# Kernel tuning notes

Hardware: AMD Instinct MI355X
Metric: run time of the kernel (lower is better)

## Reference

```python
import jax, jax.numpy as jnp
import numpy as np


def setup_inputs() -> dict:
    key = jax.random.key(0)
    x = jax.random.normal(key, (4, 4096, 64), dtype=jnp.float32)
    return {"x": x}


def reference(x) -> jnp.ndarray:
    # self-attention with q = k = v = x, shape [B, S, D]
    d = x.shape[-1]
    scale = 1.0 / jnp.sqrt(jnp.asarray(d, dtype=x.dtype))
    logits = jnp.einsum('bqd,bkd->bqk', x, x) * scale  # [B, S, S]
    attn = jax.nn.softmax(logits, axis=-1)
    return jnp.einsum('bqk,bkd->bqd', attn, x)
```

## Files before the change

kernel.cpp:

```cpp
#include <hip/hip_runtime.h>
#include <cstdint>


#define SB 4096
#define DDIM 64

typedef __attribute__((ext_vector_type(16))) float f32x16;
typedef __attribute__((ext_vector_type(8)))  float f32x8;
typedef __attribute__((ext_vector_type(4)))  float f32x4;
typedef __attribute__((ext_vector_type(8)))  short bf16x8;

static __device__ __forceinline__ unsigned short bf16_rne(float f) {
  union { float f; uint32_t u; } v; v.f = f;
  uint32_t u = v.u + 0x7FFFu + ((v.u >> 16) & 1u);
  return (unsigned short)(u >> 16);
}
static __device__ __forceinline__ float bf16_tof(unsigned short h) {
  union { uint32_t u; float f; } v; v.u = ((uint32_t)h) << 16;
  return v.f;
}
static __device__ __forceinline__ f32x16 MFMA(bf16x8 a, bf16x8 b, f32x16 c) {
  return __builtin_amdgcn_mfma_f32_32x32x16_bf16(a, b, c, 0, 0, 0);
}

#define KF_BYTES  (4u << 20)
#define VT_BYTES  (2u << 20)
#define WS_NEEDED (8u << 20)

__device__ __constant__ int g_koff[16] = {0,1,2,3, 8,9,10,11, 4,5,6,7, 12,13,14,15};

__global__ __launch_bounds__(256)
void precompute_kernel(const float* __restrict__ x, char* __restrict__ ws) {
  const int bid = blockIdx.x;
  const int tid = threadIdx.x;
  char* __restrict__ kfmt = ws;
  char* __restrict__ vthi = ws + KF_BYTES;
  char* __restrict__ vtlo = ws + KF_BYTES + VT_BYTES;
  if (bid < 512) {
    const int t   = bid * 256 + tid;
    const int row = t >> 3;
    const int seg = t & 7;
    f32x8 v = *(const f32x8*)(x + (size_t)row * 64 + seg * 8);
    bf16x8 h, l;
#pragma unroll
    for (int j = 0; j < 8; ++j) {
      unsigned short hi = bf16_rne(v[j]);
      h[j] = (short)hi;
      l[j] = (short)bf16_rne(v[j] - bf16_tof(hi));
    }
    char* dst = kfmt + (size_t)row * 256 + seg * 16;
    *(bf16x8*)dst         = h;
    *(bf16x8*)(dst + 128) = l;
  } else {
    const int w = (bid - 512) * 4 + (tid >> 6);
    const int b = w >> 8;
    const int c = w & 255;
    const int d = tid & 63;
    unsigned short hs[16], ls[16];
#pragma unroll
    for (int s = 0; s < 16; ++s) {
      const int k = c * 16 + g_koff[s];
      float v = x[((size_t)(b * SB + k)) * 64 + d];
      hs[s] = bf16_rne(v);
      ls[s] = bf16_rne(v - bf16_tof(hs[s]));
    }
    bf16x8 h0, h1, l0, l1;
#pragma unroll
    for (int j = 0; j < 8; ++j) {
      h0[j] = (short)hs[j];     h1[j] = (short)hs[j + 8];
      l0[j] = (short)ls[j];     l1[j] = (short)ls[j + 8];
    }
    char* dh = vthi + (size_t)(b * 64 + d) * 8192 + c * 32;
    char* dl = vtlo + (size_t)(b * 64 + d) * 8192 + c * 32;
    *(bf16x8*)dh = h0; *(bf16x8*)(dh + 16) = h1;
    *(bf16x8*)dl = l0; *(bf16x8*)(dl + 16) = l1;
  }
}

__global__ __launch_bounds__(512, 2)
void sdpa_main(const float* __restrict__ x, const char* __restrict__ ws,
               float* __restrict__ out) {
  __shared__ __align__(16) char smem[121856];
  const int tid  = threadIdx.x;
  const int wv   = tid >> 6;
  const int lane = tid & 63;
  const int l31  = lane & 31;
  const int h5   = lane >> 5;

  const int p    = blockIdx.x;
  const int xcd  = p & 7;
  const int slot = p >> 3;
  const int b    = xcd >> 1;
  const int q0   = ((xcd & 1) * 32 + slot) * 64;

  const float* __restrict__ xb = x + (size_t)b * (SB * DDIM);
  const char* __restrict__ kfmt = ws;
  const char* __restrict__ vthi = ws + KF_BYTES;
  const char* __restrict__ vtlo = ws + KF_BYTES + VT_BYTES;

  const float NEG = -3.0e38f;

  bf16x8 qh[2][4], ql[2][4];
#pragma unroll
  for (int qf = 0; qf < 2; ++qf) {
#pragma unroll
    for (int dc = 0; dc < 4; ++dc) {
      const float* ptr = xb + (size_t)(q0 + qf * 32 + l31) * DDIM + dc * 16 + h5 * 8;
      f32x4 a = *(const f32x4*)ptr;
      f32x4 c = *(const f32x4*)(ptr + 4);
      float v[8] = {a[0], a[1], a[2], a[3], c[0], c[1], c[2], c[3]};
#pragma unroll
      for (int j = 0; j < 8; ++j) {
        float sv = v[j] * 0.125f;
        unsigned short hi = bf16_rne(sv);
        qh[qf][dc][j] = (short)hi;
        ql[qf][dc][j] = (short)bf16_rne(sv - bf16_tof(hi));
      }
    }
  }

  f32x16 ot[2][2] = {};
  float mrun[2] = {NEG, NEG};
  float lrun[2] = {0.f, 0.f};

  const int kv0 = wv * (SB / 8);

  const char* kbase = kfmt + (size_t)(b * SB + kv0 + l31) * 256 + h5 * 16;
  const char* vbh   = vthi + (size_t)(b * 64 + l31) * 8192 + (size_t)kv0 * 2 + h5 * 16;
  const char* vbl   = vtlo + (size_t)(b * 64 + l31) * 8192 + (size_t)kv0 * 2 + h5 * 16;

#pragma unroll 1
  for (int st = 0; st < 16; ++st) {
    bf16x8 kh[4], kl[4];
#pragma unroll
    for (int dc = 0; dc < 4; ++dc) {
      kh[dc] = *(const bf16x8*)(kbase + dc * 32);
      kl[dc] = *(const bf16x8*)(kbase + 128 + dc * 32);
    }

    f32x16 s0 = {}, s1 = {};
#pragma unroll
    for (int dc = 0; dc < 4; ++dc) {
      s0 = MFMA(kh[dc], qh[0][dc], s0);
      s1 = MFMA(kh[dc], qh[1][dc], s1);
      s0 = MFMA(kh[dc], ql[0][dc], s0);
      s1 = MFMA(kh[dc], ql[1][dc], s1);
      s0 = MFMA(kl[dc], qh[0][dc], s0);
      s1 = MFMA(kl[dc], qh[1][dc], s1);
    }

    bf16x8 vh[2][2], vl[2][2];
#pragma unroll
    for (int df = 0; df < 2; ++df)
#pragma unroll
      for (int c = 0; c < 2; ++c) {
        vh[df][c] = *(const bf16x8*)(vbh + (size_t)df * (32 * 8192) + c * 32);
        vl[df][c] = *(const bf16x8*)(vbl + (size_t)df * (32 * 8192) + c * 32);
      }

    bf16x8 ph[2][2], pl[2][2];
#pragma unroll
    for (int qf = 0; qf < 2; ++qf) {
      f32x16 sv = qf ? s1 : s0;
      float pm = sv[0];
#pragma unroll
      for (int r = 1; r < 16; ++r) pm = fmaxf(pm, sv[r]);
      pm = fmaxf(pm, __shfl_xor(pm, 32));
      const float mnew = fmaxf(mrun[qf], pm);
      const float corr = __expf(mrun[qf] - mnew);
      mrun[qf] = mnew;
      lrun[qf] *= corr;
#pragma unroll
      for (int df = 0; df < 2; ++df)
#pragma unroll
        for (int r = 0; r < 16; ++r) ot[qf][df][r] *= corr;
      float pv[16]; float ps = 0.f;
#pragma unroll
      for (int r = 0; r < 16; ++r) { pv[r] = __expf(sv[r] - mnew); ps += pv[r]; }
      lrun[qf] += ps;
#pragma unroll
      for (int c = 0; c < 2; ++c)
#pragma unroll
        for (int j = 0; j < 8; ++j) {
          float pvv = pv[c * 8 + j];
          unsigned short hi = bf16_rne(pvv);
          ph[qf][c][j] = (short)hi;
          pl[qf][c][j] = (short)bf16_rne(pvv - bf16_tof(hi));
        }
    }

#pragma unroll
    for (int df = 0; df < 2; ++df)
#pragma unroll
      for (int qf = 0; qf < 2; ++qf)
#pragma unroll
        for (int c = 0; c < 2; ++c) {
          ot[qf][df] = MFMA(vh[df][c], ph[qf][c], ot[qf][df]);
          ot[qf][df] = MFMA(vh[df][c], pl[qf][c], ot[qf][df]);
          ot[qf][df] = MFMA(vl[df][c], ph[qf][c], ot[qf][df]);
        }

    kbase += 32 * 256;
    vbh   += 64;
    vbl   += 64;
  }

#pragma unroll
  for (int qf = 0; qf < 2; ++qf) lrun[qf] += __shfl_xor(lrun[qf], 32);

  __syncthreads();
  if (wv > 0) {
    char* rbase = smem + (size_t)(wv - 1) * 17408 + (size_t)lane * 272;
#pragma unroll
    for (int qf = 0; qf < 2; ++qf)
#pragma unroll
      for (int df = 0; df < 2; ++df)
#pragma unroll
        for (int t = 0; t < 4; ++t) {
          f32x4 o = { ot[qf][df][t*4+0], ot[qf][df][t*4+1],
                      ot[qf][df][t*4+2], ot[qf][df][t*4+3] };
          *(f32x4*)(rbase + (qf * 128 + df * 64 + t * 16)) = o;
        }
    f32x4 stv = { mrun[0], lrun[0], mrun[1], lrun[1] };
    *(f32x4*)(rbase + 256) = stv;
  }
  __syncthreads();
  if (wv == 0) {
#pragma unroll 1
    for (int w = 1; w < 8; ++w) {
      char* rbase = smem + (size_t)(w - 1) * 17408 + (size_t)lane * 272;
      f32x4 stv = *(f32x4*)(rbase + 256);
#pragma unroll
      for (int qf = 0; qf < 2; ++qf) {
        const float mw = stv[qf * 2 + 0];
        const float lw = stv[qf * 2 + 1];
        const float mn = fmaxf(mrun[qf], mw);
        const float f0 = __expf(mrun[qf] - mn);
        const float f1 = __expf(mw - mn);
        mrun[qf] = mn;
        lrun[qf] = lrun[qf] * f0 + lw * f1;
#pragma unroll
        for (int df = 0; df < 2; ++df)
#pragma unroll
          for (int t = 0; t < 4; ++t) {
            f32x4 o = *(f32x4*)(rbase + (qf * 128 + df * 64 + t * 16));
#pragma unroll
            for (int e = 0; e < 4; ++e)
              ot[qf][df][t*4+e] = ot[qf][df][t*4+e] * f0 + o[e] * f1;
          }
      }
    }
#pragma unroll
    for (int qf = 0; qf < 2; ++qf) {
      const float inv = 1.0f / lrun[qf];
      const size_t rowoff = ((size_t)b * SB + q0 + qf * 32 + l31) * DDIM;
#pragma unroll
      for (int df = 0; df < 2; ++df)
#pragma unroll
        for (int t = 0; t < 4; ++t) {
          const int dbase = df * 32 + t * 8 + h5 * 4;
          f32x4 o = { ot[qf][df][t*4+0] * inv, ot[qf][df][t*4+1] * inv,
                      ot[qf][df][t*4+2] * inv, ot[qf][df][t*4+3] * inv };
          *(f32x4*)(out + rowoff + dbase) = o;
        }
    }
  }
}

#define KSTRIDE 272
#define VSTRIDE 144
#define VOFF    8704
#define WREG    17920

__global__ __launch_bounds__(512, 1)
void sdpa_fb(const float* __restrict__ x, float* __restrict__ out) {
  __shared__ __align__(16) char smem[143360];
  const int tid  = threadIdx.x;
  const int wv   = tid >> 6;
  const int lane = tid & 63;
  const int l31  = lane & 31;
  const int h5   = lane >> 5;
  const int bid  = blockIdx.x;
  const int b    = bid >> 6;
  const int q0   = (bid & 63) << 6;
  const float* __restrict__ xb = x + (size_t)b * (SB * DDIM);
  char* __restrict__ wl = smem + (size_t)wv * WREG;
  const float NEG = -3.0e38f;

  bf16x8 qh[2][4], ql[2][4];
#pragma unroll
  for (int qf = 0; qf < 2; ++qf)
#pragma unroll
    for (int dc = 0; dc < 4; ++dc) {
      const float* ptr = xb + (size_t)(q0 + qf * 32 + l31) * DDIM + dc * 16 + h5 * 8;
      f32x4 a = *(const f32x4*)ptr;
      f32x4 c = *(const f32x4*)(ptr + 4);
      float v[8] = {a[0], a[1], a[2], a[3], c[0], c[1], c[2], c[3]};
#pragma unroll
      for (int j = 0; j < 8; ++j) {
        float sv = v[j] * 0.125f;
        unsigned short hi = bf16_rne(sv);
        qh[qf][dc][j] = (short)hi;
        ql[qf][dc][j] = (short)bf16_rne(sv - bf16_tof(hi));
      }
    }

  f32x16 ot[2][2] = {};
  float mrun[2] = {NEG, NEG};
  float lrun[2] = {0.f, 0.f};
  const int kv0 = wv * (SB / 8);
  const int r0  = (lane >> 3) * 4;
  const int d0g = (lane & 7) * 8;
  const int vc  = r0 >> 4;
  const int vko = r0 & 15;
  const int vsA = ((vko >> 2) & 1) * 8 + ((vko >> 3) & 1) * 4;
  const uint32_t vcolb = (uint32_t)(vc * 16 + vsA) * 2;

#pragma unroll 1
  for (int st = 0; st < 16; ++st) {
    const int krow0 = kv0 + st * 32;
    bf16x8 hv[4], lv[4];
#pragma unroll
    for (int i = 0; i < 4; ++i) {
      f32x8 t = *(const f32x8*)(xb + (size_t)(krow0 + r0 + i) * DDIM + d0g);
#pragma unroll
      for (int j = 0; j < 8; ++j) {
        unsigned short hi = bf16_rne(t[j]);
        hv[i][j] = (short)hi;
        lv[i][j] = (short)bf16_rne(t[j] - bf16_tof(hi));
      }
      const int row = r0 + i;
      *(bf16x8*)(wl + row * KSTRIDE + d0g * 2)       = hv[i];
      *(bf16x8*)(wl + row * KSTRIDE + 128 + d0g * 2) = lv[i];
    }
#pragma unroll
    for (int dd = 0; dd < 8; ++dd) {
      const int d = d0g + dd;
      const uint32_t sw = ((uint32_t)((d >> 3) & 7)) << 4;
      char* rb = wl + VOFF + (uint32_t)d * VSTRIDE;
      short4 pa = make_short4(hv[0][dd], hv[1][dd], hv[2][dd], hv[3][dd]);
      short4 pb = make_short4(lv[0][dd], lv[1][dd], lv[2][dd], lv[3][dd]);
      *(short4*)(rb + (vcolb ^ sw))        = pa;
      *(short4*)(rb + ((64 + vcolb) ^ sw)) = pb;
    }

    bf16x8 kh[4], kl[4];
    {
      char* krow = wl + l31 * KSTRIDE;
#pragma unroll
      for (int dc = 0; dc < 4; ++dc) {
        const uint32_t off = (uint32_t)(dc * 32 + h5 * 16);
        kh[dc] = *(bf16x8*)(krow + off);
        kl[dc] = *(bf16x8*)(krow + 128 + off);
      }
    }
    f32x16 s0 = {}, s1 = {};
#pragma unroll
    for (int dc = 0; dc < 4; ++dc) {
      s0 = MFMA(kh[dc], qh[0][dc], s0);
      s1 = MFMA(kh[dc], qh[1][dc], s1);
      s0 = MFMA(kh[dc], ql[0][dc], s0);
      s1 = MFMA(kh[dc], ql[1][dc], s1);
      s0 = MFMA(kl[dc], qh[0][dc], s0);
      s1 = MFMA(kl[dc], qh[1][dc], s1);
    }

    bf16x8 ph[2][2], pl[2][2];
#pragma unroll
    for (int qf = 0; qf < 2; ++qf) {
      f32x16 sv = qf ? s1 : s0;
      float pm = sv[0];
#pragma unroll
      for (int r = 1; r < 16; ++r) pm = fmaxf(pm, sv[r]);
      pm = fmaxf(pm, __shfl_xor(pm, 32));
      const float mnew = fmaxf(mrun[qf], pm);
      const float corr = __expf(mrun[qf] - mnew);
      mrun[qf] = mnew;
      lrun[qf] *= corr;
#pragma unroll
      for (int df = 0; df < 2; ++df)
#pragma unroll
        for (int r = 0; r < 16; ++r) ot[qf][df][r] *= corr;
      float pv[16]; float ps = 0.f;
#pragma unroll
      for (int r = 0; r < 16; ++r) { pv[r] = __expf(sv[r] - mnew); ps += pv[r]; }
      lrun[qf] += ps;
#pragma unroll
      for (int c = 0; c < 2; ++c)
#pragma unroll
        for (int j = 0; j < 8; ++j) {
          float pvv = pv[c * 8 + j];
          unsigned short hi = bf16_rne(pvv);
          ph[qf][c][j] = (short)hi;
          pl[qf][c][j] = (short)bf16_rne(pvv - bf16_tof(hi));
        }
    }

#pragma unroll
    for (int df = 0; df < 2; ++df) {
      const int d = df * 32 + l31;
      char* rb = wl + VOFF + (uint32_t)d * VSTRIDE;
      const uint32_t sw = ((uint32_t)((d >> 3) & 7)) << 4;
      bf16x8 vh[2], vl2[2];
#pragma unroll
      for (int c = 0; c < 2; ++c) {
        const uint32_t off = (uint32_t)(c * 32 + h5 * 16);
        vh[c]  = *(bf16x8*)(rb + (off ^ sw));
        vl2[c] = *(bf16x8*)(rb + ((64 + off) ^ sw));
      }
#pragma unroll
      for (int qf = 0; qf < 2; ++qf)
#pragma unroll
        for (int c = 0; c < 2; ++c) {
          ot[qf][df] = MFMA(vh[c],  ph[qf][c], ot[qf][df]);
          ot[qf][df] = MFMA(vh[c],  pl[qf][c], ot[qf][df]);
          ot[qf][df] = MFMA(vl2[c], ph[qf][c], ot[qf][df]);
        }
    }
  }

#pragma unroll
  for (int qf = 0; qf < 2; ++qf) lrun[qf] += __shfl_xor(lrun[qf], 32);

  __syncthreads();
  if (wv > 0) {
    char* rbase = smem + (size_t)(wv - 1) * 17408 + (size_t)lane * 272;
#pragma unroll
    for (int qf = 0; qf < 2; ++qf)
#pragma unroll
      for (int df = 0; df < 2; ++df)
#pragma unroll
        for (int t = 0; t < 4; ++t) {
          f32x4 o = { ot[qf][df][t*4+0], ot[qf][df][t*4+1],
                      ot[qf][df][t*4+2], ot[qf][df][t*4+3] };
          *(f32x4*)(rbase + (qf * 128 + df * 64 + t * 16)) = o;
        }
    f32x4 stv = { mrun[0], lrun[0], mrun[1], lrun[1] };
    *(f32x4*)(rbase + 256) = stv;
  }
  __syncthreads();
  if (wv == 0) {
#pragma unroll 1
    for (int w = 1; w < 8; ++w) {
      char* rbase = smem + (size_t)(w - 1) * 17408 + (size_t)lane * 272;
      f32x4 stv = *(f32x4*)(rbase + 256);
#pragma unroll
      for (int qf = 0; qf < 2; ++qf) {
        const float mw = stv[qf * 2 + 0];
        const float lw = stv[qf * 2 + 1];
        const float mn = fmaxf(mrun[qf], mw);
        const float f0 = __expf(mrun[qf] - mn);
        const float f1 = __expf(mw - mn);
        mrun[qf] = mn;
        lrun[qf] = lrun[qf] * f0 + lw * f1;
#pragma unroll
        for (int df = 0; df < 2; ++df)
#pragma unroll
          for (int t = 0; t < 4; ++t) {
            f32x4 o = *(f32x4*)(rbase + (qf * 128 + df * 64 + t * 16));
#pragma unroll
            for (int e = 0; e < 4; ++e)
              ot[qf][df][t*4+e] = ot[qf][df][t*4+e] * f0 + o[e] * f1;
          }
      }
    }
#pragma unroll
    for (int qf = 0; qf < 2; ++qf) {
      const float inv = 1.0f / lrun[qf];
      const size_t rowoff = ((size_t)b * SB + q0 + qf * 32 + l31) * DDIM;
#pragma unroll
      for (int df = 0; df < 2; ++df)
#pragma unroll
        for (int t = 0; t < 4; ++t) {
          const int dbase = df * 32 + t * 8 + h5 * 4;
          f32x4 o = { ot[qf][df][t*4+0] * inv, ot[qf][df][t*4+1] * inv,
                      ot[qf][df][t*4+2] * inv, ot[qf][df][t*4+3] * inv };
          *(f32x4*)(out + rowoff + dbase) = o;
        }
    }
  }
}

extern "C" void kernel_launch(void* const* d_in, const int* in_sizes, int n_in,
                              void* d_out, int out_size, void* d_ws, size_t ws_size,
                              hipStream_t stream) {
  (void)in_sizes; (void)n_in; (void)out_size;
  const float* x = (const float*)d_in[0];
  float* o = (float*)d_out;
  if (ws_size >= (size_t)WS_NEEDED) {
    precompute_kernel<<<dim3(768), dim3(256), 0, stream>>>(x, (char*)d_ws);
    sdpa_main<<<dim3(256), dim3(512), 0, stream>>>(x, (const char*)d_ws, o);
  } else {
    sdpa_fb<<<dim3(256), dim3(512), 0, stream>>>(x, o);
  }
}
```

Baseline: 129.1 us.

## Halve per-block query tile, double grid, prefetch K and tree-reduce partials

Each block now handles 32 queries instead of 64, so the grid doubles to 512 blocks, with a smaller LDS footprint and launch bounds allowing 4 blocks per CU. This is meant to raise occupancy and let more waves hide memory latency. The main loop now prefetches the next K-hi tile, splits the score MFMAs across two accumulators, and skips the rescale when no row max changes. The cross-wave merge becomes a tree reduction in shared memory. In exchange, K/V data is reread by twice as many blocks, and the block-to-XCD mapping changes.

```diff
diff --git a/kernel.cpp b/kernel.cpp
--- a/kernel.cpp
+++ b/kernel.cpp
@@ -77,21 +77,20 @@
   }
 }
 
-__global__ __launch_bounds__(512, 2)
+__global__ __launch_bounds__(512, 4)
 void sdpa_main(const float* __restrict__ x, const char* __restrict__ ws,
                float* __restrict__ out) {
-  __shared__ __align__(16) char smem[121856];
+  __shared__ __align__(16) char smem[40960];
   const int tid  = threadIdx.x;
   const int wv   = tid >> 6;
   const int lane = tid & 63;
   const int l31  = lane & 31;
   const int h5   = lane >> 5;
 
-  const int p    = blockIdx.x;
-  const int xcd  = p & 7;
-  const int slot = p >> 3;
-  const int b    = xcd >> 1;
-  const int q0   = ((xcd & 1) * 32 + slot) * 64;
+  const int p  = blockIdx.x;
+  const int b  = (p >> 1) & 3;
+  const int qt = ((p & 1) << 6) | (p >> 3);
+  const int q0 = qt * 32;
 
   const float* __restrict__ xb = x + (size_t)b * (SB * DDIM);
   const char* __restrict__ kfmt = ws;
@@ -100,169 +99,201 @@
 
   const float NEG = -3.0e38f;
 
-  bf16x8 qh[2][4], ql[2][4];
-#pragma unroll
-  for (int qf = 0; qf < 2; ++qf) {
-#pragma unroll
-    for (int dc = 0; dc < 4; ++dc) {
-      const float* ptr = xb + (size_t)(q0 + qf * 32 + l31) * DDIM + dc * 16 + h5 * 8;
-      f32x4 a = *(const f32x4*)ptr;
-      f32x4 c = *(const f32x4*)(ptr + 4);
-      float v[8] = {a[0], a[1], a[2], a[3], c[0], c[1], c[2], c[3]};
-#pragma unroll
-      for (int j = 0; j < 8; ++j) {
-        float sv = v[j] * 0.125f;
-        unsigned short hi = bf16_rne(sv);
-        qh[qf][dc][j] = (short)hi;
-        ql[qf][dc][j] = (short)bf16_rne(sv - bf16_tof(hi));
-      }
-    }
-  }
-
-  f32x16 ot[2][2] = {};
-  float mrun[2] = {NEG, NEG};
-  float lrun[2] = {0.f, 0.f};
-
-  const int kv0 = wv * (SB / 8);
-
-  const char* kbase = kfmt + (size_t)(b * SB + kv0 + l31) * 256 + h5 * 16;
-  const char* vbh   = vthi + (size_t)(b * 64 + l31) * 8192 + (size_t)kv0 * 2 + h5 * 16;
-  const char* vbl   = vtlo + (size_t)(b * 64 + l31) * 8192 + (size_t)kv0 * 2 + h5 * 16;
+  bf16x8 qh[4], ql[4];
+#pragma unroll
+  for (int dc = 0; dc < 4; ++dc) {
+    const float* ptr = xb + (size_t)(q0 + l31) * DDIM + dc * 16 + h5 * 8;
+    f32x4 a = *(const f32x4*)ptr;
+    f32x4 c = *(const f32x4*)(ptr + 4);
+    float v[8] = {a[0], a[1], a[2], a[3], c[0], c[1], c[2], c[3]};
+#pragma unroll
+    for (int j = 0; j < 8; ++j) {
+      float sv = v[j] * 0.125f;
+      unsigned short hi = bf16_rne(sv);
+      qh[dc][j] = (short)hi;
+      ql[dc][j] = (short)bf16_rne(sv - bf16_tof(hi));
+    }
+  }
+
+  f32x16 ot0 = {}, ot1 = {};
+  float mrun = NEG, lrun = 0.f;
+
+  const int kv0 = wv * 512;
+  const int koffl = l31 * 256 + h5 * 16;
+  const int voffl = l31 * 8192 + h5 * 16;
+  const char* kstep = kfmt + (size_t)(b * SB + kv0) * 256;
+  const char* vhs   = vthi + (size_t)(b * 64) * 8192 + kv0 * 2;
+  const char* vls   = vtlo + (size_t)(b * 64) * 8192 + kv0 * 2;
+
+  bf16x8 kh[4], kl[4];
+#pragma unroll
+  for (int dc = 0; dc < 4; ++dc)
+    kh[dc] = *(const bf16x8*)(kstep + koffl + dc * 32);
 
 #pragma unroll 1
   for (int st = 0; st < 16; ++st) {
-    bf16x8 kh[4], kl[4];
+#pragma unroll
+    for (int dc = 0; dc < 4; ++dc)
+      kl[dc] = *(const bf16x8*)(kstep + koffl + 128 + dc * 32);
+
+    f32x16 sa = {}, sb = {};
 #pragma unroll
     for (int dc = 0; dc < 4; ++dc) {
-      kh[dc] = *(const bf16x8*)(kbase + dc * 32);
-      kl[dc] = *(const bf16x8*)(kbase + 128 + dc * 32);
-    }
-
-    f32x16 s0 = {}, s1 = {};
-#pragma unroll
-    for (int dc = 0; dc < 4; ++dc) {
-      s0 = MFMA(kh[dc], qh[0][dc], s0);
-      s1 = MFMA(kh[dc], qh[1][dc], s1);
-      s0 = MFMA(kh[dc], ql[0][dc], s0);
-      s1 = MFMA(kh[dc], ql[1][dc], s1);
-      s0 = MFMA(kl[dc], qh[0][dc], s0);
-      s1 = MFMA(kl[dc], qh[1][dc], s1);
-    }
-
-    bf16x8 vh[2][2], vl[2][2];
+      sa = MFMA(kh[dc], qh[dc], sa);
+      sb = MFMA(kh[dc], ql[dc], sb);
+    }
+
+    kstep += 32 * 256;
+#pragma unroll
+    for (int dc = 0; dc < 4; ++dc)
+      kh[dc] = *(const bf16x8*)(kstep + koffl + dc * 32);
+
+#pragma unroll
+    for (int dc = 0; dc < 4; ++dc)
+      sb = MFMA(kl[dc], qh[dc], sb);
+
+    float s[16];
+#pragma unroll
+    for (int r = 0; r < 16; ++r) s[r] = sa[r] + sb[r];
+
+    bf16x8 vh[2][2];
 #pragma unroll
     for (int df = 0; df < 2; ++df)
 #pragma unroll
-      for (int c = 0; c < 2; ++c) {
-        vh[df][c] = *(const bf16x8*)(vbh + (size_t)df * (32 * 8192) + c * 32);
-        vl[df][c] = *(const bf16x8*)(vbl + (size_t)df * (32 * 8192) + c * 32);
+      for (int c = 0; c < 2; ++c)
+        vh[df][c] = *(const bf16x8*)(vhs + (size_t)df * (32 * 8192) + voffl + c * 32);
+
+    float m0 = fmaxf(s[0], s[1]),  m1 = fmaxf(s[2], s[3]);
+    float m2 = fmaxf(s[4], s[5]),  m3 = fmaxf(s[6], s[7]);
+    float m4 = fmaxf(s[8], s[9]),  m5 = fmaxf(s[10], s[11]);
+    float m6 = fmaxf(s[12], s[13]), m7 = fmaxf(s[14], s[15]);
+    float a0 = fmaxf(m0, m1), a1 = fmaxf(m2, m3);
+    float a2 = fmaxf(m4, m5), a3 = fmaxf(m6, m7);
+    float pm = fmaxf(fmaxf(a0, a1), fmaxf(a2, a3));
+    pm = fmaxf(pm, __shfl_xor(pm, 32));
+
+    if (!__all(pm <= mrun)) {
+      const float mnew = fmaxf(mrun, pm);
+      const float corr = __expf(mrun - mnew);
+      mrun = mnew;
+      lrun *= corr;
+#pragma unroll
+      for (int r = 0; r < 16; ++r) { ot0[r] *= corr; ot1[r] *= corr; }
+    }
+
+#pragma unroll
+    for (int r = 0; r < 16; ++r) s[r] = __expf(s[r] - mrun);
+    {
+      float t0 = (s[0] + s[1]) + (s[2] + s[3]);
+      float t1 = (s[4] + s[5]) + (s[6] + s[7]);
+      float t2 = (s[8] + s[9]) + (s[10] + s[11]);
+      float t3 = (s[12] + s[13]) + (s[14] + s[15]);
+      lrun += (t0 + t1) + (t2 + t3);
+    }
+
+    bf16x8 ph[2], pl[2];
+#pragma unroll
+    for (int c = 0; c < 2; ++c)
+#pragma unroll
+      for (int j = 0; j < 8; ++j) {
+        float pv = s[c * 8 + j];
+        unsigned short hi = bf16_rne(pv);
+        ph[c][j] = (short)hi;
+        pl[c][j] = (short)bf16_rne(pv - bf16_tof(hi));
       }
 
-    bf16x8 ph[2][2], pl[2][2];
-#pragma unroll
-    for (int qf = 0; qf < 2; ++qf) {
-      f32x16 sv = qf ? s1 : s0;
-      float pm = sv[0];
-#pragma unroll
-      for (int r = 1; r < 16; ++r) pm = fmaxf(pm, sv[r]);
-      pm = fmaxf(pm, __shfl_xor(pm, 32));
-      const float mnew = fmaxf(mrun[qf], pm);
-      const float corr = __expf(mrun[qf] - mnew);
-      mrun[qf] = mnew;
-      lrun[qf] *= corr;
-#pragma unroll
-      for (int df = 0; df < 2; ++df)
-#pragma unroll
-        for (int r = 0; r < 16; ++r) ot[qf][df][r] *= corr;
-      float pv[16]; float ps = 0.f;
-#pragma unroll
-      for (int r = 0; r < 16; ++r) { pv[r] = __expf(sv[r] - mnew); ps += pv[r]; }
-      lrun[qf] += ps;
+    bf16x8 vl[2][2];
+#pragma unroll
+    for (int df = 0; df < 2; ++df)
 #pragma unroll
       for (int c = 0; c < 2; ++c)
-#pragma unroll
-        for (int j = 0; j < 8; ++j) {
-          float pvv = pv[c * 8 + j];
-          unsigned short hi = bf16_rne(pvv);
-          ph[qf][c][j] = (short)hi;
-          pl[qf][c][j] = (short)bf16_rne(pvv - bf16_tof(hi));
-        }
-    }
-
-#pragma unroll
-    for (int df = 0; df < 2; ++df)
-#pragma unroll
-      for (int qf = 0; qf < 2; ++qf)
-#pragma unroll
-        for (int c = 0; c < 2; ++c) {
-          ot[qf][df] = MFMA(vh[df][c], ph[qf][c], ot[qf][df]);
-          ot[qf][df] = MFMA(vh[df][c], pl[qf][c], ot[qf][df]);
-          ot[qf][df] = MFMA(vl[df][c], ph[qf][c], ot[qf][df]);
-        }
-
-    kbase += 32 * 256;
-    vbh   += 64;
-    vbl   += 64;
-  }
-
-#pragma unroll
-  for (int qf = 0; qf < 2; ++qf) lrun[qf] += __shfl_xor(lrun[qf], 32);
-
-  __syncthreads();
-  if (wv > 0) {
-    char* rbase = smem + (size_t)(wv - 1) * 17408 + (size_t)lane * 272;
-#pragma unroll
-    for (int qf = 0; qf < 2; ++qf)
-#pragma unroll
-      for (int df = 0; df < 2; ++df)
-#pragma unroll
-        for (int t = 0; t < 4; ++t) {
-          f32x4 o = { ot[qf][df][t*4+0], ot[qf][df][t*4+1],
-                      ot[qf][df][t*4+2], ot[qf][df][t*4+3] };
-          *(f32x4*)(rbase + (qf * 128 + df * 64 + t * 16)) = o;
-        }
-    f32x4 stv = { mrun[0], lrun[0], mrun[1], lrun[1] };
-    *(f32x4*)(rbase + 256) = stv;
-  }
+        vl[df][c] = *(const bf16x8*)(vls + (size_t)df * (32 * 8192) + voffl + c * 32);
+
+#pragma unroll
+    for (int c = 0; c < 2; ++c) {
+      ot0 = MFMA(vh[0][c], ph[c], ot0);
+      ot1 = MFMA(vh[1][c], ph[c], ot1);
+      ot0 = MFMA(vh[0][c], pl[c], ot0);
+      ot1 = MFMA(vh[1][c], pl[c], ot1);
+    }
+#pragma unroll
+    for (int c = 0; c < 2; ++c) {
+      ot0 = MFMA(vl[0][c], ph[c], ot0);
+      ot1 = MFMA(vl[1][c], ph[c], ot1);
+    }
+
+    vhs += 64;
+    vls += 64;
+  }
+
+  lrun += __shfl_xor(lrun, 32);
+
+  auto writeR = [&](int r) {
+    char* bse = smem + r * 10240 + lane * 160;
+#pragma unroll
+    for (int t = 0; t < 4; ++t) {
+      f32x4 o = { ot0[t*4+0], ot0[t*4+1], ot0[t*4+2], ot0[t*4+3] };
+      *(f32x4*)(bse + t * 16) = o;
+    }
+#pragma unroll
+    for (int t = 0; t < 4; ++t) {
+      f32x4 o = { ot1[t*4+0], ot1[t*4+1], ot1[t*4+2], ot1[t*4+3] };
+      *(f32x4*)(bse + 64 + t * 16) = o;
+    }
+    f32x4 stv = { mrun, lrun, 0.f, 0.f };
+    *(f32x4*)(bse + 128) = stv;
+  };
+  auto mergeR = [&](int r) {
+    char* bse = smem + r * 10240 + lane * 160;
+    f32x4 stv = *(f32x4*)(bse + 128);
+    const float mw = stv[0], lw = stv[1];
+    const float mn = fmaxf(mrun, mw);
+    const float f0 = __expf(mrun - mn);
+    const float f1 = __expf(mw - mn);
+    mrun = mn;
+    lrun = lrun * f0 + lw * f1;
+#pragma unroll
+    for (int t = 0; t < 4; ++t) {
+      f32x4 o = *(f32x4*)(bse + t * 16);
+#pragma unroll
+      for (int e = 0; e < 4; ++e) ot0[t*4+e] = ot0[t*4+e] * f0 + o[e] * f1;
+    }
+#pragma unroll
+    for (int t = 0; t < 4; ++t) {
+      f32x4 o = *(f32x4*)(bse + 64 + t * 16);
+#pragma unroll
+      for (int e = 0; e < 4; ++e) ot1[t*4+e] = ot1[t*4+e] * f0 + o[e] * f1;
+    }
+  };
+
+  __syncthreads();
+  if (wv >= 4) writeR(wv - 4);
+  __syncthreads();
+  if (wv < 4) mergeR(wv);
+  __syncthreads();
+  if (wv == 2 || wv == 3) writeR(wv - 2);
+  __syncthreads();
+  if (wv < 2) mergeR(wv);
+  __syncthreads();
+  if (wv == 1) writeR(0);
   __syncthreads();
   if (wv == 0) {
-#pragma unroll 1
-    for (int w = 1; w < 8; ++w) {
-      char* rbase = smem + (size_t)(w - 1) * 17408 + (size_t)lane * 272;
-      f32x4 stv = *(f32x4*)(rbase + 256);
-#pragma unroll
-      for (int qf = 0; qf < 2; ++qf) {
-        const float mw = stv[qf * 2 + 0];
-        const float lw = stv[qf * 2 + 1];
-        const float mn = fmaxf(mrun[qf], mw);
-        const float f0 = __expf(mrun[qf] - mn);
-        const float f1 = __expf(mw - mn);
-        mrun[qf] = mn;
-        lrun[qf] = lrun[qf] * f0 + lw * f1;
-#pragma unroll
-        for (int df = 0; df < 2; ++df)
-#pragma unroll
-          for (int t = 0; t < 4; ++t) {
-            f32x4 o = *(f32x4*)(rbase + (qf * 128 + df * 64 + t * 16));
-#pragma unroll
-            for (int e = 0; e < 4; ++e)
-              ot[qf][df][t*4+e] = ot[qf][df][t*4+e] * f0 + o[e] * f1;
-          }
-      }
-    }
-#pragma unroll
-    for (int qf = 0; qf < 2; ++qf) {
-      const float inv = 1.0f / lrun[qf];
-      const size_t rowoff = ((size_t)b * SB + q0 + qf * 32 + l31) * DDIM;
-#pragma unroll
-      for (int df = 0; df < 2; ++df)
-#pragma unroll
-        for (int t = 0; t < 4; ++t) {
-          const int dbase = df * 32 + t * 8 + h5 * 4;
-          f32x4 o = { ot[qf][df][t*4+0] * inv, ot[qf][df][t*4+1] * inv,
-                      ot[qf][df][t*4+2] * inv, ot[qf][df][t*4+3] * inv };
-          *(f32x4*)(out + rowoff + dbase) = o;
-        }
+    mergeR(0);
+    const float inv = 1.0f / lrun;
+    const size_t rowoff = ((size_t)b * SB + q0 + l31) * DDIM;
+#pragma unroll
+    for (int t = 0; t < 4; ++t) {
+      const int dbase = t * 8 + h5 * 4;
+      f32x4 o = { ot0[t*4+0] * inv, ot0[t*4+1] * inv,
+                  ot0[t*4+2] * inv, ot0[t*4+3] * inv };
+      *(f32x4*)(out + rowoff + dbase) = o;
+    }
+#pragma unroll
+    for (int t = 0; t < 4; ++t) {
+      const int dbase = 32 + t * 8 + h5 * 4;
+      f32x4 o = { ot1[t*4+0] * inv, ot1[t*4+1] * inv,
+                  ot1[t*4+2] * inv, ot1[t*4+3] * inv };
+      *(f32x4*)(out + rowoff + dbase) = o;
     }
   }
 }
@@ -489,7 +520,7 @@
   float* o = (float*)d_out;
   if (ws_size >= (size_t)WS_NEEDED) {
     precompute_kernel<<<dim3(768), dim3(256), 0, stream>>>(x, (char*)d_ws);
-    sdpa_main<<<dim3(256), dim3(512), 0, stream>>>(x, (const char*)d_ws, o);
+    sdpa_main<<<dim3(512), dim3(512), 0, stream>>>(x, (const char*)d_ws, o);
   } else {
     sdpa_fb<<<dim3(256), dim3(512), 0, stream>>>(x, o);
   }
```

New measurement: 219.5 us. +70.0%, slower.
